# Optimization experiments

Measured on AMD Instinct MI355X. Metric: run time of the kernel, lower is better.

## Reference

```python
import jax, jax.numpy as jnp
import numpy as np

N_NODES = 50000
N_EDGES = 800000
F_IN, HID, N_CLS = 128, 64, 40
KS = 2  # kernel_size, dim=1, open B-spline, degree=1


def spline_conv(x, src, dst, pseudo, W, root, bias, num_nodes, kernel_size):
    """SplineConv (torch_geometric), dim=1, degree=1, open spline, aggr='mean'."""
    K = kernel_size
    v = pseudo[:, 0] * (K - 1)                       # map [0,1] -> [0, K-1]
    k0 = jnp.clip(jnp.floor(v), 0, K - 2)
    frac = v - k0                                    # linear (degree-1) basis
    i0 = k0.astype(jnp.int32)
    i1 = i0 + 1
    E = src.shape[0]
    e = jnp.arange(E)
    # per-edge kernel coefficients c[e,k] = sum_s basis[e,s]*[idx[e,s]==k]
    c = jnp.zeros((E, K), x.dtype).at[e, i0].add(1.0 - frac).at[e, i1].add(frac)
    xj = x[src]                                      # [E, F_in] gather
    # agg[k] = scatter-add over edges of c[e,k]*xj[e] -> [K, N, F_in]
    agg = jnp.stack([
        jax.ops.segment_sum(c[:, k:k + 1] * xj, dst, num_segments=num_nodes)
        for k in range(K)
    ])
    deg = jax.ops.segment_sum(jnp.ones((E,), x.dtype), dst, num_segments=num_nodes)
    msg = jnp.einsum('kni,kio->no', agg, W) / jnp.maximum(deg, 1.0)[:, None]
    return msg + x @ root + bias


def setup_inputs() -> dict:
    key = jax.random.key(0)
    ks = jax.random.split(key, 9)
    def glorot(k, shape):
        fan_in, fan_out = shape[-2], shape[-1]
        lim = (6.0 / (fan_in + fan_out)) ** 0.5
        return jax.random.uniform(k, shape, jnp.float32, -lim, lim)
    return {
        'x': jax.random.normal(ks[0], (N_NODES, F_IN), jnp.float32),
        'edge_index': jax.random.randint(ks[1], (2, N_EDGES), 0, N_NODES, jnp.int32),
        'edge_attr': jax.random.uniform(ks[2], (N_EDGES, 1), jnp.float32),
        'W1': glorot(ks[3], (KS, F_IN, HID)),
        'root1': glorot(ks[4], (F_IN, HID)),
        'bias1': jnp.zeros((HID,), jnp.float32),
        'W2': glorot(ks[5], (KS, HID, N_CLS)),
        'root2': glorot(ks[6], (HID, N_CLS)),
        'bias2': jnp.zeros((N_CLS,), jnp.float32),
    }


def reference(x, edge_index, edge_attr, W1, root1, bias1, W2, root2, bias2):
    src, dst = edge_index[0], edge_index[1]
    # eval mode: dropout is identity
    h = spline_conv(x, src, dst, edge_attr, W1, root1, bias1, N_NODES, KS)
    h = jax.nn.elu(h)
    out = spline_conv(h, src, dst, edge_attr, W2, root2, bias2, N_NODES, KS)
    return out
```

## Files before the change

### kernel.cpp

```cpp
#include <hip/hip_runtime.h>
#include <math.h>

#define N_NODES 50000
#define N_EDGES 800000
#define F_IN    128
#define HID     64
#define N_CLS   40

#define M1 (3 * HID)
#define M2P 128

#define RANGE_SZ 6250
#define PERM_SLICES 128
#define PERM_CHUNK (N_EDGES / PERM_SLICES)
#define EST 64

#define NW 32768

using sh8 = __attribute__((ext_vector_type(8))) short;
using floatx4 = __attribute__((ext_vector_type(4))) float;

__device__ inline unsigned short f2bf(float f) {
    union { float f; unsigned int u; } c{f};
    unsigned int r = (c.u + 0x7FFF + ((c.u >> 16) & 1)) >> 16;
    return (unsigned short)r;
}
__device__ inline float bf2f(unsigned int u) {
    union { unsigned int u; float f; } c;
    c.u = u << 16;
    return c.f;
}

__global__ void concat_w(const float* __restrict__ W1, const float* __restrict__ root1,
                         const float* __restrict__ W2, const float* __restrict__ root2,
                         unsigned short* __restrict__ WT1, unsigned short* __restrict__ WT2,
                         int* __restrict__ cnt) {
    int i = blockIdx.x * blockDim.x + threadIdx.x;
    if (i < M1 * F_IN) {
        int c = i / F_IN, k = i % F_IN;
        float val;
        if (c < HID)            val = W1[k * HID + c];
        else if (c < 2 * HID)   val = W1[F_IN * HID + k * HID + (c - HID)];
        else                    val = root1[k * HID + (c - 2 * HID)];
        WT1[i] = f2bf(val);
    } else if (i < NW) {
        int ii = i - M1 * F_IN;
        int c = ii / HID, k = ii % HID;
        float val;
        if (c < N_CLS)            val = W2[k * N_CLS + c];
        else if (c < 2 * N_CLS)   val = W2[HID * N_CLS + k * N_CLS + (c - N_CLS)];
        else if (c < 3 * N_CLS)   val = root2[k * N_CLS + (c - 2 * N_CLS)];
        else                      val = 0.0f;
        WT2[ii] = f2bf(val);
    } else {
        int ii = i - NW;
        if (ii < N_NODES) cnt[ii] = 0;
    }
}

template <int KD, bool AF32, int SPLIT, int PW, int ROOTW, int MT>
__device__ __forceinline__ void gemm_body(int bid, const void* __restrict__ Aptr,
                                          const unsigned short* __restrict__ Bt,
                                          unsigned short* __restrict__ Csp,
                                          float* __restrict__ Croot, int Crows) {
    constexpr int KP = KD + 8;
    __shared__ unsigned short As[64 * KP];
    __shared__ unsigned short Bs[64 * KP];

    int tid = threadIdx.x;
    int row0 = bid * 64;

    if (AF32) {
        const float* A = (const float*)Aptr;
        for (int c = tid; c < 64 * (KD / 4); c += 256) {
            int r = c / (KD / 4), q = c % (KD / 4);
            int gr = row0 + r;
            float4 v = make_float4(0.f, 0.f, 0.f, 0.f);
            if (gr < Crows) v = *(const float4*)(A + (size_t)gr * KD + q * 4);
            union { unsigned short s[4]; uint2 u; } pk;
            pk.s[0] = f2bf(v.x); pk.s[1] = f2bf(v.y);
            pk.s[2] = f2bf(v.z); pk.s[3] = f2bf(v.w);
            *(uint2*)&As[r * KP + q * 4] = pk.u;
        }
    } else {
        const unsigned short* A = (const unsigned short*)Aptr;
        for (int c = tid; c < 64 * (KD / 8); c += 256) {
            int r = c / (KD / 8), q = c % (KD / 8);
            int gr = row0 + r;
            sh8 v = {};
            if (gr < Crows) v = *(const sh8*)(A + (size_t)gr * KD + q * 8);
            *(sh8*)&As[r * KP + q * 8] = v;
        }
    }

    int wv = tid >> 6, lane = tid & 63;
    int lrow = lane & 15, lq = lane >> 4;

    for (int mt = 0; mt < MT; ++mt) {
        int c0 = mt * 64;
        __syncthreads();
        for (int c = tid; c < 64 * (KD / 8); c += 256) {
            int r = c / (KD / 8), q = c % (KD / 8);
            *(sh8*)&Bs[r * KP + q * 8] = *(const sh8*)(Bt + (size_t)(c0 + r) * KD + q * 8);
        }
        __syncthreads();

        floatx4 acc[4] = {{0.f,0.f,0.f,0.f},{0.f,0.f,0.f,0.f},{0.f,0.f,0.f,0.f},{0.f,0.f,0.f,0.f}};
#pragma unroll
        for (int kt = 0; kt < KD / 32; ++kt) {
            int kb = kt * 32 + lq * 8;
            sh8 a0 = *(const sh8*)&As[(wv * 16 + lrow) * KP + kb];
#pragma unroll
            for (int cf = 0; cf < 4; ++cf) {
                sh8 b = *(const sh8*)&Bs[(cf * 16 + lrow) * KP + kb];
                acc[cf] = __builtin_amdgcn_mfma_f32_16x16x32_bf16(a0, b, acc[cf], 0, 0, 0);
            }
        }

#pragma unroll
        for (int r = 0; r < 4; ++r) {
            int gr = row0 + wv * 16 + lq * 4 + r;
            if (gr >= Crows) continue;
#pragma unroll
            for (int cf = 0; cf < 4; ++cf) {
                int gc = c0 + cf * 16 + lrow;
                float val = acc[cf][r];
                if (gc < SPLIT) {
                    int pi = (gc < PW) ? gc * 2 : (gc - PW) * 2 + 1;
                    Csp[(size_t)gr * SPLIT + pi] = f2bf(val);
                } else if (gc < SPLIT + ROOTW) {
                    Croot[(size_t)gr * ROOTW + (gc - SPLIT)] = val;
                }
            }
        }
    }
}

__device__ __forceinline__ void permute_body(int b, const int* __restrict__ src,
                                             const int* __restrict__ dst,
                                             const float* __restrict__ attr,
                                             int* __restrict__ cnt,
                                             unsigned int* __restrict__ edata) {
    int range = b & 7;
    int slice = b >> 3;
    int lo = range * RANGE_SZ;
    int e0 = slice * PERM_CHUNK;
    int e1 = e0 + PERM_CHUNK;
    for (int e = e0 + (int)threadIdx.x; e < e1; e += 256) {
        int d = dst[e];
        if ((unsigned)(d - lo) < (unsigned)RANGE_SZ) {
            int pos = atomicAdd(&cnt[d], 1);
            if (pos < EST) {
                unsigned int q = (unsigned int)(attr[e] * 65535.0f + 0.5f);
                edata[d * EST + pos] = (unsigned int)src[e] | (q << 16);
            }
        }
    }
}

__global__ __launch_bounds__(256) void gemm1_permute(const float* __restrict__ x,
                                                     const unsigned short* __restrict__ WT1,
                                                     unsigned short* __restrict__ Ysp,
                                                     float* __restrict__ Yroot,
                                                     const int* __restrict__ src,
                                                     const int* __restrict__ dst,
                                                     const float* __restrict__ attr,
                                                     int* __restrict__ cnt,
                                                     unsigned int* __restrict__ edata,
                                                     int gemmBlocks) {
    if ((int)blockIdx.x < gemmBlocks) {
        gemm_body<128, true, 128, 64, 64, 3>(blockIdx.x, (const void*)x, WT1, Ysp, Yroot, N_NODES);
    } else {
        permute_body(blockIdx.x - gemmBlocks, src, dst, attr, cnt, edata);
    }
}

template <int KD, bool AF32, int SPLIT, int PW, int ROOTW, int MT>
__global__ __launch_bounds__(256) void gemm_mfma(const void* __restrict__ Aptr,
                                                 const unsigned short* __restrict__ Bt,
                                                 unsigned short* __restrict__ Csp,
                                                 float* __restrict__ Croot,
                                                 int Crows) {
    gemm_body<KD, AF32, SPLIT, PW, ROOTW, MT>(blockIdx.x, Aptr, Bt, Csp, Croot, Crows);
}

__global__ __launch_bounds__(256) void gather1(const unsigned short* __restrict__ Ysp,
                                               const float* __restrict__ Yroot,
                                               const int* __restrict__ cnt,
                                               const unsigned int* __restrict__ edata,
                                               const float* __restrict__ bias1,
                                               unsigned short* __restrict__ h) {
    int wave = (blockIdx.x * blockDim.x + threadIdx.x) >> 6;
    int lane = threadIdx.x & 63;
    if (wave >= N_NODES) return;
    int hf = lane >> 5;
    int c  = lane & 31;
    int deg = cnt[wave];
    deg = deg > EST ? EST : deg;
    const unsigned int* eb = edata + (size_t)wave * EST;
    const float qs = 1.0f / 65535.0f;
    float a0 = 0.0f, a1 = 0.0f;
    if (deg <= 16) {
        unsigned int e[8]; uint2 p[8];
#pragma unroll
        for (int t = 0; t < 8; ++t) e[t] = eb[2 * t + hf];
#pragma unroll
        for (int t = 0; t < 8; ++t) {
            int idx = (2 * t + hf < deg) ? (int)(e[t] & 0xffffu) : 0;
            p[t] = *(const uint2*)(Ysp + (size_t)idx * 128 + c * 4);
        }
#pragma unroll
        for (int t = 0; t < 8; ++t) {
            float m = (2 * t + hf < deg) ? 1.0f : 0.0f;
            float v = (float)(e[t] >> 16) * qs;
            float w = 1.0f - v;
            a0 += m * (w * bf2f(p[t].x & 0xffffu) + v * bf2f(p[t].x >> 16));
            a1 += m * (w * bf2f(p[t].y & 0xffffu) + v * bf2f(p[t].y >> 16));
        }
    } else {
        unsigned int e[16]; uint2 p[16];
#pragma unroll
        for (int t = 0; t < 16; ++t) e[t] = eb[2 * t + hf];
#pragma unroll
        for (int t = 0; t < 16; ++t) {
            int idx = (2 * t + hf < deg) ? (int)(e[t] & 0xffffu) : 0;
            p[t] = *(const uint2*)(Ysp + (size_t)idx * 128 + c * 4);
        }
#pragma unroll
        for (int t = 0; t < 16; ++t) {
            float m = (2 * t + hf < deg) ? 1.0f : 0.0f;
            float v = (float)(e[t] >> 16) * qs;
            float w = 1.0f - v;
            a0 += m * (w * bf2f(p[t].x & 0xffffu) + v * bf2f(p[t].x >> 16));
            a1 += m * (w * bf2f(p[t].y & 0xffffu) + v * bf2f(p[t].y >> 16));
        }
        if (deg > 32) {
            for (int j = 32 + hf; j < deg; j += 2) {
                unsigned int ee = eb[j];
                int idx = (int)(ee & 0xffffu);
                uint2 pp = *(const uint2*)(Ysp + (size_t)idx * 128 + c * 4);
                float v = (float)(ee >> 16) * qs;
                float w = 1.0f - v;
                a0 += w * bf2f(pp.x & 0xffffu) + v * bf2f(pp.x >> 16);
                a1 += w * bf2f(pp.y & 0xffffu) + v * bf2f(pp.y >> 16);
            }
        }
    }
    a0 += __shfl_xor(a0, 32);
    a1 += __shfl_xor(a1, 32);
    float dg = (float)deg;
    dg = dg > 1.0f ? dg : 1.0f;
    float2 yr = *(const float2*)(Yroot + (size_t)wave * HID + c * 2);
    float2 bi = *(const float2*)(bias1 + c * 2);
    float m0 = a0 / dg + yr.x + bi.x;
    float m1 = a1 / dg + yr.y + bi.y;
    m0 = m0 > 0.0f ? m0 : expm1f(m0);
    m1 = m1 > 0.0f ? m1 : expm1f(m1);
    if (hf == 0) {
        unsigned int u = (unsigned int)f2bf(m0) | ((unsigned int)f2bf(m1) << 16);
        *(unsigned int*)(h + (size_t)wave * HID + c * 2) = u;
    }
}

__global__ __launch_bounds__(256) void gather2(const unsigned short* __restrict__ Zsp,
                                               const float* __restrict__ Zroot,
                                               const int* __restrict__ cnt,
                                               const unsigned int* __restrict__ edata,
                                               const float* __restrict__ bias2,
                                               float* __restrict__ out) {
    int wave = (blockIdx.x * blockDim.x + threadIdx.x) >> 6;
    int lane = threadIdx.x & 63;
    if (wave >= N_NODES) return;
    int hf = lane >> 5;
    int c  = lane & 31;
    int deg = cnt[wave];
    deg = deg > EST ? EST : deg;
    const unsigned int* eb = edata + (size_t)wave * EST;
    const float qs = 1.0f / 65535.0f;
    float a0 = 0.0f, a1 = 0.0f;
    if (c < 20) {
        if (deg <= 16) {
            unsigned int e[8]; uint2 p[8];
#pragma unroll
            for (int t = 0; t < 8; ++t) e[t] = eb[2 * t + hf];
#pragma unroll
            for (int t = 0; t < 8; ++t) {
                int idx = (2 * t + hf < deg) ? (int)(e[t] & 0xffffu) : 0;
                p[t] = *(const uint2*)(Zsp + (size_t)idx * 80 + c * 4);
            }
#pragma unroll
            for (int t = 0; t < 8; ++t) {
                float m = (2 * t + hf < deg) ? 1.0f : 0.0f;
                float v = (float)(e[t] >> 16) * qs;
                float w = 1.0f - v;
                a0 += m * (w * bf2f(p[t].x & 0xffffu) + v * bf2f(p[t].x >> 16));
                a1 += m * (w * bf2f(p[t].y & 0xffffu) + v * bf2f(p[t].y >> 16));
            }
        } else {
            unsigned int e[16]; uint2 p[16];
#pragma unroll
            for (int t = 0; t < 16; ++t) e[t] = eb[2 * t + hf];
#pragma unroll
            for (int t = 0; t < 16; ++t) {
                int idx = (2 * t + hf < deg) ? (int)(e[t] & 0xffffu) : 0;
                p[t] = *(const uint2*)(Zsp + (size_t)idx * 80 + c * 4);
            }
#pragma unroll
            for (int t = 0; t < 16; ++t) {
                float m = (2 * t + hf < deg) ? 1.0f : 0.0f;
                float v = (float)(e[t] >> 16) * qs;
                float w = 1.0f - v;
                a0 += m * (w * bf2f(p[t].x & 0xffffu) + v * bf2f(p[t].x >> 16));
                a1 += m * (w * bf2f(p[t].y & 0xffffu) + v * bf2f(p[t].y >> 16));
            }
            if (deg > 32) {
                for (int j = 32 + hf; j < deg; j += 2) {
                    unsigned int ee = eb[j];
                    int idx = (int)(ee & 0xffffu);
                    uint2 pp = *(const uint2*)(Zsp + (size_t)idx * 80 + c * 4);
                    float v = (float)(ee >> 16) * qs;
                    float w = 1.0f - v;
                    a0 += w * bf2f(pp.x & 0xffffu) + v * bf2f(pp.x >> 16);
                    a1 += w * bf2f(pp.y & 0xffffu) + v * bf2f(pp.y >> 16);
                }
            }
        }
    }
    a0 += __shfl_xor(a0, 32);
    a1 += __shfl_xor(a1, 32);
    if (hf == 0 && c < 20) {
        float dg = (float)deg;
        dg = dg > 1.0f ? dg : 1.0f;
        float2 zr = *(const float2*)(Zroot + (size_t)wave * N_CLS + c * 2);
        float2 bi = *(const float2*)(bias2 + c * 2);
        float2 o;
        o.x = a0 / dg + zr.x + bi.x;
        o.y = a1 / dg + zr.y + bi.y;
        *(float2*)(out + (size_t)wave * N_CLS + c * 2) = o;
    }
}

extern "C" void kernel_launch(void* const* d_in, const int* in_sizes, int n_in,
                              void* d_out, int out_size, void* d_ws, size_t ws_size,
                              hipStream_t stream) {
    const float* x     = (const float*)d_in[0];
    const int*   eidx  = (const int*)d_in[1];
    const float* eattr = (const float*)d_in[2];
    const float* W1    = (const float*)d_in[3];
    const float* root1 = (const float*)d_in[4];
    const float* bias1 = (const float*)d_in[5];
    const float* W2    = (const float*)d_in[6];
    const float* root2 = (const float*)d_in[7];
    const float* bias2 = (const float*)d_in[8];
    float* out = (float*)d_out;

    const int* src = eidx;
    const int* dst = eidx + N_EDGES;

    char* base = (char*)d_ws;
    unsigned short* Ysp   = (unsigned short*)base;
    float*          Yroot = (float*)(base + 12800000);
    unsigned short* hb    = (unsigned short*)(base + 25600000);
    unsigned short* WT1   = (unsigned short*)(base + 32000000);
    unsigned short* WT2   = (unsigned short*)(base + 32049152);
    unsigned int*   edata = (unsigned int*)(base + 32065536);
    int*            cnt   = (int*)(base + 44865536);
    unsigned short* Zsp   = Ysp;
    float*          Zroot = Yroot;

    const int GB = (N_NODES + 63) / 64;

    hipLaunchKernelGGL(concat_w, dim3((NW + N_NODES + 255) / 256), dim3(256), 0, stream,
                       W1, root1, W2, root2, WT1, WT2, cnt);

    hipLaunchKernelGGL(gemm1_permute, dim3(GB + 8 * PERM_SLICES), dim3(256), 0, stream,
                       x, WT1, Ysp, Yroot, src, dst, eattr, cnt, edata, GB);
    hipLaunchKernelGGL(gather1, dim3((N_NODES * 64 + 255) / 256), dim3(256), 0, stream,
                       Ysp, Yroot, cnt, edata, bias1, hb);

    hipLaunchKernelGGL((gemm_mfma<64, false, 80, 40, 40, 2>),
                       dim3(GB), dim3(256), 0, stream,
                       (const void*)hb, WT2, Zsp, Zroot, N_NODES);
    hipLaunchKernelGGL(gather2, dim3((N_NODES * 64 + 255) / 256), dim3(256), 0, stream,
                       Zsp, Zroot, cnt, edata, bias2, out);
}
```

Before: 200.4 us.

## Reorder layer 2 to aggregate before transform, then one fused GEMM

Layer 2 now gathers and aggregates the 64-wide bf16 hidden features per spline kernel into a [N,192] buffer (two aggregated halves plus h copied alongside) and then runs a single K=192 MFMA GEMM that writes the output with bias. Before, it ran a GEMM to a 120-wide projection and then gathered 80-wide bf16 rows per edge. The per-edge gather now reads 128 bytes per edge instead of 160. In exchange it adds an extra 19 MB write and read of the A192 buffer, and the aggregated means are rounded to bf16 before the GEMM, which changes numerics.

```diff
diff --git a/kernel.cpp b/kernel.cpp
--- a/kernel.cpp
+++ b/kernel.cpp
@@ -8,14 +8,14 @@
 #define N_CLS   40
 
 #define M1 (3 * HID)
-#define M2P 128
+#define K2  192
 
 #define RANGE_SZ 6250
 #define PERM_SLICES 128
 #define PERM_CHUNK (N_EDGES / PERM_SLICES)
 #define EST 64
 
-#define NW 32768
+#define NW (M1 * F_IN + N_CLS * K2)
 
 using sh8 = __attribute__((ext_vector_type(8))) short;
 using floatx4 = __attribute__((ext_vector_type(4))) float;
@@ -45,12 +45,11 @@
         WT1[i] = f2bf(val);
     } else if (i < NW) {
         int ii = i - M1 * F_IN;
-        int c = ii / HID, k = ii % HID;
+        int c = ii / K2, k = ii % K2;
         float val;
-        if (c < N_CLS)            val = W2[k * N_CLS + c];
-        else if (c < 2 * N_CLS)   val = W2[HID * N_CLS + k * N_CLS + (c - N_CLS)];
-        else if (c < 3 * N_CLS)   val = root2[k * N_CLS + (c - 2 * N_CLS)];
-        else                      val = 0.0f;
+        if (k < HID)             val = W2[k * N_CLS + c];
+        else if (k < 2 * HID)    val = W2[HID * N_CLS + (k - HID) * N_CLS + c];
+        else                     val = root2[(k - 2 * HID) * N_CLS + c];
         WT2[ii] = f2bf(val);
     } else {
         int ii = i - NW;
@@ -175,21 +174,13 @@
     }
 }
 
-template <int KD, bool AF32, int SPLIT, int PW, int ROOTW, int MT>
-__global__ __launch_bounds__(256) void gemm_mfma(const void* __restrict__ Aptr,
-                                                 const unsigned short* __restrict__ Bt,
-                                                 unsigned short* __restrict__ Csp,
-                                                 float* __restrict__ Croot,
-                                                 int Crows) {
-    gemm_body<KD, AF32, SPLIT, PW, ROOTW, MT>(blockIdx.x, Aptr, Bt, Csp, Croot, Crows);
-}
-
 __global__ __launch_bounds__(256) void gather1(const unsigned short* __restrict__ Ysp,
                                                const float* __restrict__ Yroot,
                                                const int* __restrict__ cnt,
                                                const unsigned int* __restrict__ edata,
                                                const float* __restrict__ bias1,
-                                               unsigned short* __restrict__ h) {
+                                               unsigned short* __restrict__ h,
+                                               unsigned short* __restrict__ A192) {
     int wave = (blockIdx.x * blockDim.x + threadIdx.x) >> 6;
     int lane = threadIdx.x & 63;
     if (wave >= N_NODES) return;
@@ -259,15 +250,14 @@
     if (hf == 0) {
         unsigned int u = (unsigned int)f2bf(m0) | ((unsigned int)f2bf(m1) << 16);
         *(unsigned int*)(h + (size_t)wave * HID + c * 2) = u;
-    }
-}
-
-__global__ __launch_bounds__(256) void gather2(const unsigned short* __restrict__ Zsp,
-                                               const float* __restrict__ Zroot,
-                                               const int* __restrict__ cnt,
-                                               const unsigned int* __restrict__ edata,
-                                               const float* __restrict__ bias2,
-                                               float* __restrict__ out) {
+        *(unsigned int*)(A192 + (size_t)wave * K2 + 128 + c * 2) = u;
+    }
+}
+
+__global__ __launch_bounds__(256) void gather2h(const unsigned short* __restrict__ hb,
+                                                const int* __restrict__ cnt,
+                                                const unsigned int* __restrict__ edata,
+                                                unsigned short* __restrict__ A192) {
     int wave = (blockIdx.x * blockDim.x + threadIdx.x) >> 6;
     int lane = threadIdx.x & 63;
     if (wave >= N_NODES) return;
@@ -277,66 +267,123 @@
     deg = deg > EST ? EST : deg;
     const unsigned int* eb = edata + (size_t)wave * EST;
     const float qs = 1.0f / 65535.0f;
-    float a0 = 0.0f, a1 = 0.0f;
-    if (c < 20) {
-        if (deg <= 16) {
-            unsigned int e[8]; uint2 p[8];
-#pragma unroll
-            for (int t = 0; t < 8; ++t) e[t] = eb[2 * t + hf];
-#pragma unroll
-            for (int t = 0; t < 8; ++t) {
-                int idx = (2 * t + hf < deg) ? (int)(e[t] & 0xffffu) : 0;
-                p[t] = *(const uint2*)(Zsp + (size_t)idx * 80 + c * 4);
-            }
-#pragma unroll
-            for (int t = 0; t < 8; ++t) {
-                float m = (2 * t + hf < deg) ? 1.0f : 0.0f;
-                float v = (float)(e[t] >> 16) * qs;
+    float a00 = 0.0f, a01 = 0.0f, a10 = 0.0f, a11 = 0.0f;
+    if (deg <= 16) {
+        unsigned int e[8], p[8];
+#pragma unroll
+        for (int t = 0; t < 8; ++t) e[t] = eb[2 * t + hf];
+#pragma unroll
+        for (int t = 0; t < 8; ++t) {
+            int idx = (2 * t + hf < deg) ? (int)(e[t] & 0xffffu) : 0;
+            p[t] = *(const unsigned int*)(hb + (size_t)idx * HID + c * 2);
+        }
+#pragma unroll
+        for (int t = 0; t < 8; ++t) {
+            float m = (2 * t + hf < deg) ? 1.0f : 0.0f;
+            float v = (float)(e[t] >> 16) * qs;
+            float wm = m * (1.0f - v), vm = m * v;
+            float h0 = bf2f(p[t] & 0xffffu), h1 = bf2f(p[t] >> 16);
+            a00 += wm * h0; a01 += wm * h1;
+            a10 += vm * h0; a11 += vm * h1;
+        }
+    } else {
+        unsigned int e[16], p[16];
+#pragma unroll
+        for (int t = 0; t < 16; ++t) e[t] = eb[2 * t + hf];
+#pragma unroll
+        for (int t = 0; t < 16; ++t) {
+            int idx = (2 * t + hf < deg) ? (int)(e[t] & 0xffffu) : 0;
+            p[t] = *(const unsigned int*)(hb + (size_t)idx * HID + c * 2);
+        }
+#pragma unroll
+        for (int t = 0; t < 16; ++t) {
+            float m = (2 * t + hf < deg) ? 1.0f : 0.0f;
+            float v = (float)(e[t] >> 16) * qs;
+            float wm = m * (1.0f - v), vm = m * v;
+            float h0 = bf2f(p[t] & 0xffffu), h1 = bf2f(p[t] >> 16);
+            a00 += wm * h0; a01 += wm * h1;
+            a10 += vm * h0; a11 += vm * h1;
+        }
+        if (deg > 32) {
+            for (int j = 32 + hf; j < deg; j += 2) {
+                unsigned int ee = eb[j];
+                int idx = (int)(ee & 0xffffu);
+                unsigned int pp = *(const unsigned int*)(hb + (size_t)idx * HID + c * 2);
+                float v = (float)(ee >> 16) * qs;
                 float w = 1.0f - v;
-                a0 += m * (w * bf2f(p[t].x & 0xffffu) + v * bf2f(p[t].x >> 16));
-                a1 += m * (w * bf2f(p[t].y & 0xffffu) + v * bf2f(p[t].y >> 16));
-            }
-        } else {
-            unsigned int e[16]; uint2 p[16];
-#pragma unroll
-            for (int t = 0; t < 16; ++t) e[t] = eb[2 * t + hf];
-#pragma unroll
-            for (int t = 0; t < 16; ++t) {
-                int idx = (2 * t + hf < deg) ? (int)(e[t] & 0xffffu) : 0;
-                p[t] = *(const uint2*)(Zsp + (size_t)idx * 80 + c * 4);
-            }
-#pragma unroll
-            for (int t = 0; t < 16; ++t) {
-                float m = (2 * t + hf < deg) ? 1.0f : 0.0f;
-                float v = (float)(e[t] >> 16) * qs;
-                float w = 1.0f - v;
-                a0 += m * (w * bf2f(p[t].x & 0xffffu) + v * bf2f(p[t].x >> 16));
-                a1 += m * (w * bf2f(p[t].y & 0xffffu) + v * bf2f(p[t].y >> 16));
-            }
-            if (deg > 32) {
-                for (int j = 32 + hf; j < deg; j += 2) {
-                    unsigned int ee = eb[j];
-                    int idx = (int)(ee & 0xffffu);
-                    uint2 pp = *(const uint2*)(Zsp + (size_t)idx * 80 + c * 4);
-                    float v = (float)(ee >> 16) * qs;
-                    float w = 1.0f - v;
-                    a0 += w * bf2f(pp.x & 0xffffu) + v * bf2f(pp.x >> 16);
-                    a1 += w * bf2f(pp.y & 0xffffu) + v * bf2f(pp.y >> 16);
-                }
-            }
-        }
-    }
-    a0 += __shfl_xor(a0, 32);
-    a1 += __shfl_xor(a1, 32);
-    if (hf == 0 && c < 20) {
+                float h0 = bf2f(pp & 0xffffu), h1 = bf2f(pp >> 16);
+                a00 += w * h0; a01 += w * h1;
+                a10 += v * h0; a11 += v * h1;
+            }
+        }
+    }
+    a00 += __shfl_xor(a00, 32);
+    a01 += __shfl_xor(a01, 32);
+    a10 += __shfl_xor(a10, 32);
+    a11 += __shfl_xor(a11, 32);
+    if (hf == 0) {
         float dg = (float)deg;
         dg = dg > 1.0f ? dg : 1.0f;
-        float2 zr = *(const float2*)(Zroot + (size_t)wave * N_CLS + c * 2);
-        float2 bi = *(const float2*)(bias2 + c * 2);
-        float2 o;
-        o.x = a0 / dg + zr.x + bi.x;
-        o.y = a1 / dg + zr.y + bi.y;
-        *(float2*)(out + (size_t)wave * N_CLS + c * 2) = o;
+        float inv = 1.0f / dg;
+        unsigned int u0 = (unsigned int)f2bf(a00 * inv) | ((unsigned int)f2bf(a01 * inv) << 16);
+        unsigned int u1 = (unsigned int)f2bf(a10 * inv) | ((unsigned int)f2bf(a11 * inv) << 16);
+        *(unsigned int*)(A192 + (size_t)wave * K2 + c * 2) = u0;
+        *(unsigned int*)(A192 + (size_t)wave * K2 + 64 + c * 2) = u1;
+    }
+}
+
+__global__ __launch_bounds__(256) void gemm_out(const unsigned short* __restrict__ A,
+                                                const unsigned short* __restrict__ Bt,
+                                                const float* __restrict__ bias2,
+                                                float* __restrict__ out) {
+    constexpr int KD = K2, KP = KD + 8;
+    __shared__ unsigned short As[64 * KP];
+    __shared__ unsigned short Bs[64 * KP];
+
+    int tid = threadIdx.x;
+    int row0 = blockIdx.x * 64;
+
+    for (int c = tid; c < 64 * (KD / 8); c += 256) {
+        int r = c / (KD / 8), q = c % (KD / 8);
+        int gr = row0 + r;
+        sh8 v = {};
+        if (gr < N_NODES) v = *(const sh8*)(A + (size_t)gr * KD + q * 8);
+        *(sh8*)&As[r * KP + q * 8] = v;
+    }
+    for (int c = tid; c < 64 * (KD / 8); c += 256) {
+        int r = c / (KD / 8), q = c % (KD / 8);
+        sh8 v = {};
+        if (r < N_CLS) v = *(const sh8*)(Bt + (size_t)r * KD + q * 8);
+        *(sh8*)&Bs[r * KP + q * 8] = v;
+    }
+    __syncthreads();
+
+    int wv = tid >> 6, lane = tid & 63;
+    int lrow = lane & 15, lq = lane >> 4;
+
+    floatx4 acc[4] = {{0.f,0.f,0.f,0.f},{0.f,0.f,0.f,0.f},{0.f,0.f,0.f,0.f},{0.f,0.f,0.f,0.f}};
+#pragma unroll
+    for (int kt = 0; kt < KD / 32; ++kt) {
+        int kb = kt * 32 + lq * 8;
+        sh8 a0 = *(const sh8*)&As[(wv * 16 + lrow) * KP + kb];
+#pragma unroll
+        for (int cf = 0; cf < 4; ++cf) {
+            sh8 b = *(const sh8*)&Bs[(cf * 16 + lrow) * KP + kb];
+            acc[cf] = __builtin_amdgcn_mfma_f32_16x16x32_bf16(a0, b, acc[cf], 0, 0, 0);
+        }
+    }
+
+#pragma unroll
+    for (int r = 0; r < 4; ++r) {
+        int gr = row0 + wv * 16 + lq * 4 + r;
+        if (gr >= N_NODES) continue;
+#pragma unroll
+        for (int cf = 0; cf < 4; ++cf) {
+            int gc = cf * 16 + lrow;
+            if (gc < N_CLS) {
+                out[(size_t)gr * N_CLS + gc] = acc[cf][r] + bias2[gc];
+            }
+        }
     }
 }
 
@@ -365,8 +412,7 @@
     unsigned short* WT2   = (unsigned short*)(base + 32049152);
     unsigned int*   edata = (unsigned int*)(base + 32065536);
     int*            cnt   = (int*)(base + 44865536);
-    unsigned short* Zsp   = Ysp;
-    float*          Zroot = Yroot;
+    unsigned short* A192  = (unsigned short*)(base + 45065536);
 
     const int GB = (N_NODES + 63) / 64;
 
@@ -375,12 +421,13 @@
 
     hipLaunchKernelGGL(gemm1_permute, dim3(GB + 8 * PERM_SLICES), dim3(256), 0, stream,
                        x, WT1, Ysp, Yroot, src, dst, eattr, cnt, edata, GB);
+
     hipLaunchKernelGGL(gather1, dim3((N_NODES * 64 + 255) / 256), dim3(256), 0, stream,
-                       Ysp, Yroot, cnt, edata, bias1, hb);
-
-    hipLaunchKernelGGL((gemm_mfma<64, false, 80, 40, 40, 2>),
-                       dim3(GB), dim3(256), 0, stream,
-                       (const void*)hb, WT2, Zsp, Zroot, N_NODES);
-    hipLaunchKernelGGL(gather2, dim3((N_NODES * 64 + 255) / 256), dim3(256), 0, stream,
-                       Zsp, Zroot, cnt, edata, bias2, out);
-}
+                       Ysp, Yroot, cnt, edata, bias1, hb, A192);
+
+    hipLaunchKernelGGL(gather2h, dim3((N_NODES * 64 + 255) / 256), dim3(256), 0, stream,
+                       hb, cnt, edata, A192);
+
+    hipLaunchKernelGGL(gemm_out, dim3(GB), dim3(256), 0, stream,
+                       A192, WT2, bias2, out);
+}
```

After: 198.2 us. Within noise of the previous version (-1.1%).
